# Kernel tuning notes

Hardware: AMD Instinct MI355X
Metric: run time of the kernel (lower is better)

## Reference

```python
import jax, jax.numpy as jnp
import numpy as np

H, W = 128, 128
TANX, TANY = 0.5, 0.5
SCALE_MOD = 1.0
N = 2048
T_EPS = 1e-4          # early-termination threshold used by the CUDA kernel
ALPHA_MIN = 1.0 / 255.0


def setup_inputs() -> dict:
    key = jax.random.key(0)
    ks = jax.random.split(key, 6)
    z = jax.random.uniform(ks[0], (N,), minval=2.0, maxval=6.0)
    xy = jax.random.uniform(ks[1], (N, 2), minval=-0.8, maxval=0.8) * (z[:, None] * TANX)
    means3D = jnp.concatenate([xy, z[:, None]], axis=1).astype(jnp.float32)
    means2D = jnp.zeros((N, 3), jnp.float32)  # gradient receptacle in the original API
    opacities = (jax.random.uniform(ks[2], (N, 1)) * 0.9 + 0.05).astype(jnp.float32)
    colors_precomp = jax.random.uniform(ks[3], (N, 3)).astype(jnp.float32)
    scales = jax.random.uniform(ks[4], (N, 3), minval=0.01, maxval=0.05).astype(jnp.float32)
    q = jax.random.normal(ks[5], (N, 4))
    rotations = (q / jnp.linalg.norm(q, axis=1, keepdims=True)).astype(jnp.float32)
    bg = jnp.zeros((3,), jnp.float32)
    viewmatrix = jnp.eye(4, dtype=jnp.float32)  # camera at origin looking +z (row-vector convention)
    znear, zfar = 0.01, 100.0
    P = np.zeros((4, 4), np.float32)
    P[0, 0] = 1.0 / TANX
    P[1, 1] = 1.0 / TANY
    P[2, 2] = zfar / (zfar - znear)
    P[2, 3] = -(zfar * znear) / (zfar - znear)
    P[3, 2] = 1.0
    projmatrix = jnp.asarray(P.T)  # full view@proj, row-vector convention
    return dict(bg=bg, means3D=means3D, means2D=means2D, opacities=opacities,
                colors_precomp=colors_precomp, scales=scales, rotations=rotations,
                viewmatrix=viewmatrix, projmatrix=projmatrix)


def _quat_to_rot(q):
    r, x, y, z = q[:, 0], q[:, 1], q[:, 2], q[:, 3]
    return jnp.stack([
        jnp.stack([1 - 2 * (y * y + z * z), 2 * (x * y - r * z), 2 * (x * z + r * y)], -1),
        jnp.stack([2 * (x * y + r * z), 1 - 2 * (x * x + z * z), 2 * (y * z - r * x)], -1),
        jnp.stack([2 * (x * z - r * y), 2 * (y * z + r * x), 1 - 2 * (x * x + y * y)], -1)], -2)


def _rasterize(bg, means3D, opacities, colors, scales, rotations, viewmatrix, projmatrix):
    n = means3D.shape[0]
    mh = jnp.concatenate([means3D, jnp.ones((n, 1), means3D.dtype)], 1)
    p_view = mh @ viewmatrix                 # [N,4] camera-space position
    tz = p_view[:, 2]
    p_hom = mh @ projmatrix
    p_proj = p_hom[:, :3] / (p_hom[:, 3:4] + 1e-7)
    # 3D covariance Sigma = (R S)(R S)^T
    qn = rotations / jnp.linalg.norm(rotations, axis=1, keepdims=True)
    Rm = _quat_to_rot(qn)
    M = Rm * (scales * SCALE_MOD)[:, None, :]      # R @ diag(s)
    Sigma = jnp.einsum('nij,nkj->nik', M, M)
    # EWA projection to a 2D covariance
    fx, fy = W / (2 * TANX), H / (2 * TANY)
    tx = jnp.clip(p_view[:, 0] / tz, -1.3 * TANX, 1.3 * TANX) * tz
    ty = jnp.clip(p_view[:, 1] / tz, -1.3 * TANY, 1.3 * TANY) * tz
    zero = jnp.zeros_like(tz)
    J = jnp.stack([jnp.stack([fx / tz, zero, -fx * tx / (tz * tz)], -1),
                   jnp.stack([zero, fy / tz, -fy * ty / (tz * tz)], -1)], -2)  # [N,2,3]
    Wr = viewmatrix[:3, :3]
    cov_cam = jnp.einsum('ji,njk,kl->nil', Wr, Sigma, Wr)      # W^T Sigma W
    cov2d = jnp.einsum('nij,njk,nlk->nil', J, cov_cam, J)      # [N,2,2]
    a = cov2d[:, 0, 0] + 0.3
    c = cov2d[:, 1, 1] + 0.3
    b = cov2d[:, 0, 1]
    det = a * c - b * b
    valid = (tz > 0.2) & (det > 0.0)                            # near-plane + degenerate culling
    det_s = jnp.where(det > 0.0, det, 1.0)
    conA, conB, conC = c / det_s, -b / det_s, a / det_s         # conic (inverse 2D cov)
    mid = 0.5 * (a + c)
    lam = mid + jnp.sqrt(jnp.maximum(0.1, mid * mid - det))
    radii = jnp.where(valid, jnp.ceil(3.0 * jnp.sqrt(lam)), 0.0).astype(jnp.int32)
    # NDC -> pixel coords
    px = ((p_proj[:, 0] + 1.0) * W - 1.0) * 0.5
    py = ((p_proj[:, 1] + 1.0) * H - 1.0) * 0.5
    # global front-to-back depth sort (per-tile in the CUDA kernel)
    order = jnp.argsort(tz)
    px_s, py_s = px[order], py[order]
    cA, cB, cC = conA[order], conB[order], conC[order]
    op_s = opacities[order, 0]
    col_s = colors[order]
    tz_s = tz[order]
    val_s = valid[order]
    yy, xx = jnp.meshgrid(jnp.arange(H, dtype=means3D.dtype),
                          jnp.arange(W, dtype=means3D.dtype), indexing='ij')
    gx, gy = xx.reshape(-1, 1), yy.reshape(-1, 1)   # [P,1]
    dx = px_s[None, :] - gx                          # [P,N]
    dy = py_s[None, :] - gy
    power = -0.5 * (cA[None, :] * dx * dx + cC[None, :] * dy * dy) - cB[None, :] * dx * dy
    alpha = jnp.minimum(0.99, op_s[None, :] * jnp.exp(power))
    alpha = jnp.where((power <= 0.0) & (alpha >= ALPHA_MIN) & val_s[None, :], alpha, 0.0)
    Tinc = jnp.cumprod(1.0 - alpha, axis=1)
    T = jnp.concatenate([jnp.ones((H * W, 1), alpha.dtype), Tinc[:, :-1]], axis=1)  # exclusive transmittance
    wgt = jnp.where(T > T_EPS, alpha * T, 0.0)       # early termination
    color = wgt @ col_s + Tinc[:, -1:] * bg[None, :]  # [P,3]
    depth = wgt @ tz_s                                # [P]
    counter = jnp.sum(wgt > 0.0, axis=1).astype(jnp.int32)
    color = color.reshape(H, W, 3).transpose(2, 0, 1)
    depth = depth.reshape(1, H, W)
    counter = counter.reshape(H, W)
    return color, depth, radii, counter


def reference(bg, means3D, means2D, opacities, colors_precomp, scales, rotations, viewmatrix, projmatrix):
    # means2D is only a gradient receptacle in the original API; it does not affect the math.
    return _rasterize(bg, means3D, opacities, colors_precomp, scales, rotations, viewmatrix, projmatrix)
```

## Files before the change

kernel.cpp:

```cpp
#include <hip/hip_runtime.h>
#include <math.h>

#define N_G   2048
#define W_IMG 128
#define H_IMG 128
#define NPIX  (W_IMG * H_IMG)
#define TANX  0.5f
#define TANY  0.5f
#define ALPHA_MIN (1.0f / 255.0f)
#define T_EPS_C 1e-4f
#define NTHR  1024
#define NWAVE 16
#define CAP   1024

__device__ __forceinline__ void full_chain(int i,
        const float* __restrict__ means3D, const float* __restrict__ opac,
        const float* __restrict__ colors, const float* __restrict__ scales,
        const float* __restrict__ rots, const float* __restrict__ viewm,
        const float* __restrict__ projm,
        float4& f1, float4& f2, float& radf) {
    float mx = means3D[i * 3 + 0], my = means3D[i * 3 + 1], mz = means3D[i * 3 + 2];
    float pv0 = mx * viewm[0] + my * viewm[4] + mz * viewm[8]  + viewm[12];
    float pv1 = mx * viewm[1] + my * viewm[5] + mz * viewm[9]  + viewm[13];
    float tz  = mx * viewm[2] + my * viewm[6] + mz * viewm[10] + viewm[14];

    float qr = rots[i * 4 + 0], qx = rots[i * 4 + 1], qy = rots[i * 4 + 2], qz = rots[i * 4 + 3];
    float qn = __builtin_amdgcn_rsqf(qr * qr + qx * qx + qy * qy + qz * qz);
    qr *= qn; qx *= qn; qy *= qn; qz *= qn;
    float R[3][3] = {
        {1.0f - 2.0f * (qy * qy + qz * qz), 2.0f * (qx * qy - qr * qz), 2.0f * (qx * qz + qr * qy)},
        {2.0f * (qx * qy + qr * qz), 1.0f - 2.0f * (qx * qx + qz * qz), 2.0f * (qy * qz - qr * qx)},
        {2.0f * (qx * qz - qr * qy), 2.0f * (qy * qz + qr * qx), 1.0f - 2.0f * (qx * qx + qy * qy)}};

    float sc[3] = {scales[i * 3 + 0], scales[i * 3 + 1], scales[i * 3 + 2]};
    float M[3][3];
#pragma unroll
    for (int r = 0; r < 3; r++)
#pragma unroll
        for (int cx = 0; cx < 3; cx++) M[r][cx] = R[r][cx] * sc[cx];

    float Sg[3][3];
#pragma unroll
    for (int r = 0; r < 3; r++)
#pragma unroll
        for (int kk = 0; kk < 3; kk++)
            Sg[r][kk] = M[r][0] * M[kk][0] + M[r][1] * M[kk][1] + M[r][2] * M[kk][2];

    float T1[3][3];
#pragma unroll
    for (int j = 0; j < 3; j++)
#pragma unroll
        for (int l = 0; l < 3; l++)
            T1[j][l] = Sg[j][0] * viewm[0 * 4 + l] + Sg[j][1] * viewm[1 * 4 + l] + Sg[j][2] * viewm[2 * 4 + l];
    float Cc[3][3];
#pragma unroll
    for (int r = 0; r < 3; r++)
#pragma unroll
        for (int l = 0; l < 3; l++)
            Cc[r][l] = viewm[0 * 4 + r] * T1[0][l] + viewm[1 * 4 + r] * T1[1][l] + viewm[2 * 4 + r] * T1[2][l];

    const float fx = W_IMG / (2.0f * TANX), fy = H_IMG / (2.0f * TANY);
    float invtz = __builtin_amdgcn_rcpf(tz);
    float txl = fminf(fmaxf(pv0 * invtz, -1.3f * TANX), 1.3f * TANX) * tz;
    float tyl = fminf(fmaxf(pv1 * invtz, -1.3f * TANY), 1.3f * TANY) * tz;
    float a0 = fx * invtz, a2 = -fx * txl * invtz * invtz;
    float b1 = fy * invtz, b2 = -fy * tyl * invtz * invtz;

    float c00 = a0 * a0 * Cc[0][0] + 2.0f * a0 * a2 * Cc[0][2] + a2 * a2 * Cc[2][2];
    float c11 = b1 * b1 * Cc[1][1] + 2.0f * b1 * b2 * Cc[1][2] + b2 * b2 * Cc[2][2];
    float c01 = a0 * b1 * Cc[0][1] + a0 * b2 * Cc[0][2] + a2 * b1 * Cc[1][2] + a2 * b2 * Cc[2][2];

    float a = c00 + 0.3f, c = c11 + 0.3f, b = c01;
    float det = a * c - b * b;
    bool valid = (tz > 0.2f) && (det > 0.0f);
    float det_s = (det > 0.0f) ? det : 1.0f;
    float rdet = __builtin_amdgcn_rcpf(det_s);
    float conA = c * rdet, conB = -b * rdet, conC = a * rdet;
    float mid = 0.5f * (a + c);
    float lam = mid + __builtin_amdgcn_sqrtf(fmaxf(0.1f, mid * mid - det));
    radf = valid ? ceilf(3.0f * __builtin_amdgcn_sqrtf(lam)) : 0.0f;

    float op = opac[i];
    f1 = make_float4(conA, conB, conC, valid ? op : 0.0f);
    f2 = make_float4(colors[i * 3 + 0], colors[i * 3 + 1], colors[i * 3 + 2], tz);
}

__global__ __launch_bounds__(NTHR) void gs_fused(const float* __restrict__ means3D,
                                                 const float* __restrict__ opac,
                                                 const float* __restrict__ colors,
                                                 const float* __restrict__ scales,
                                                 const float* __restrict__ rots,
                                                 const float* __restrict__ viewm,
                                                 const float* __restrict__ projm,
                                                 const float* __restrict__ bg,
                                                 float* __restrict__ out) {
    __shared__ float4 bbx[N_G];
    __shared__ float  tzv[N_G];
    __shared__ unsigned short lst[N_G];
    __shared__ float4 sf1[CAP];
    __shared__ float4 sf2[CAP];
    __shared__ float2 spos[CAP];
    __shared__ float4 scratch4[CAP / 4];
    __shared__ float4 accv[NTHR];
    __shared__ int s_count;

    float* scr = (float*)scratch4;
    int tid = threadIdx.x;
    int bid = blockIdx.x;
    float* radii_out = out + 4 * NPIX;
    if (tid == 0) s_count = 0;

    float cs0 = fabsf(viewm[0]) + fabsf(viewm[4]) + fabsf(viewm[8]);
    float cs1 = fabsf(viewm[1]) + fabsf(viewm[5]) + fabsf(viewm[9]);
    float cs2 = fabsf(viewm[2]) + fabsf(viewm[6]) + fabsf(viewm[10]);
    float rs0 = fabsf(viewm[0]) + fabsf(viewm[1]) + fabsf(viewm[2]);
    float rs1 = fabsf(viewm[4]) + fabsf(viewm[5]) + fabsf(viewm[6]);
    float rs2 = fabsf(viewm[8]) + fabsf(viewm[9]) + fabsf(viewm[10]);
    float wb2 = fmaxf(cs0, fmaxf(cs1, cs2)) * fmaxf(rs0, fmaxf(rs1, rs2));

#pragma unroll
    for (int k = 0; k < N_G / NTHR; k++) {
        int i = k * NTHR + tid;
        float mx = means3D[i * 3 + 0], my = means3D[i * 3 + 1], mz = means3D[i * 3 + 2];
        float pv0 = mx * viewm[0] + my * viewm[4] + mz * viewm[8]  + viewm[12];
        float pv1 = mx * viewm[1] + my * viewm[5] + mz * viewm[9]  + viewm[13];
        float tz  = mx * viewm[2] + my * viewm[6] + mz * viewm[10] + viewm[14];

        float ph[4];
#pragma unroll
        for (int j = 0; j < 4; j++)
            ph[j] = mx * projm[0 * 4 + j] + my * projm[1 * 4 + j] + mz * projm[2 * 4 + j] + projm[3 * 4 + j];
        float inv_w = __builtin_amdgcn_rcpf(ph[3] + 1e-7f);
        float px = ((ph[0] * inv_w + 1.0f) * (float)W_IMG - 1.0f) * 0.5f;
        float py = ((ph[1] * inv_w + 1.0f) * (float)H_IMG - 1.0f) * 0.5f;

        float s0 = scales[i * 3 + 0], s1 = scales[i * 3 + 1], s2 = scales[i * 3 + 2];
        float smax2 = fmaxf(s0 * s0, fmaxf(s1 * s1, s2 * s2));
        float op = opac[i];
        float L = __logf(255.0f * op);

        float invtz = __builtin_amdgcn_rcpf(tz);
        float ux = pv0 * invtz, uy = pv1 * invtz;
        float u2x = fminf(ux * ux, 0.4225f);
        float u2y = fminf(uy * uy, 0.4225f);
        float f2 = (W_IMG / (2.0f * TANX)) * invtz;
        f2 *= f2;
        float sw = smax2 * wb2;
        float abound = f2 * (1.0f + u2x) * sw + 0.3f;
        float cbound = f2 * (1.0f + u2y) * sw + 0.3f;
        float exb = __builtin_amdgcn_sqrtf(2.0f * L * abound) * 1.03f + 0.05f;
        float eyb = __builtin_amdgcn_sqrtf(2.0f * L * cbound) * 1.03f + 0.05f;
        if (!(tz > 0.2f) || !(L > 0.0f)) { exb = -1e9f; eyb = -1e9f; }

        bbx[i] = make_float4(px, py, exb, eyb);
        tzv[i] = tz;
    }
    __syncthreads();

    int tilex = bid & 15, tiley = bid >> 4;
    int wave = tid >> 6, lane = tid & 63;

    {
        float tx0 = (float)(tilex << 3), ty0 = (float)(tiley << 3);
        float tx1 = tx0 + 7.0f, ty1 = ty0 + 7.0f;
#pragma unroll
        for (int cc = 0; cc < 2; cc++) {
            int gi = (wave * 2 + cc) * 64 + lane;
            float4 b = bbx[gi];
            bool pred = (b.x >= tx0 - b.z) && (b.x <= tx1 + b.z) &&
                        (b.y >= ty0 - b.w) && (b.y <= ty1 + b.w);
            unsigned long long m = __ballot(pred);
            int n = (int)__popcll(m);
            int base = 0;
            if (lane == 0 && n) base = atomicAdd(&s_count, n);
            base = __shfl(base, 0);
            if (pred)
                lst[base + (int)__popcll(m & ((1ull << lane) - 1ull))] = (unsigned short)gi;
        }
    }
    __syncthreads();
    int c = min(s_count, CAP);

    for (int t = tid; t < c; t += NTHR) scr[t] = tzv[lst[t]];
    __syncthreads();

    for (int t = tid; t < c; t += NTHR) {
        int gi = lst[t];
        float my = scr[t];
        int rank = 0;
        int j = 0;
        for (; j + 4 <= c; j += 4) {
            float4 v = scratch4[j >> 2];
            int i0 = lst[j], i1 = lst[j + 1], i2 = lst[j + 2], i3 = lst[j + 3];
            rank += (v.x < my) || (v.x == my && i0 < gi);
            rank += (v.y < my) || (v.y == my && i1 < gi);
            rank += (v.z < my) || (v.z == my && i2 < gi);
            rank += (v.w < my) || (v.w == my && i3 < gi);
        }
        for (; j < c; j++) {
            float v = scr[j];
            rank += (v < my) || (v == my && lst[j] < gi);
        }
        float4 f1, f2v; float radf;
        full_chain(gi, means3D, opac, colors, scales, rots, viewm, projm, f1, f2v, radf);
        sf1[rank] = f1;
        sf2[rank] = f2v;
        float4 b = bbx[gi];
        spos[rank] = make_float2(b.x, b.y);
    }
    if (tid < 8) {
        int g8 = bid * 8 + tid;
        float4 d1, d2; float radf;
        full_chain(g8, means3D, opac, colors, scales, rots, viewm, projm, d1, d2, radf);
        radii_out[g8] = (float)(int)radf;
    }
    __syncthreads();

    float gx = (float)((tilex << 3) + (lane & 7));
    float gy = (float)((tiley << 3) + (lane >> 3));
    int seglen = (c + NWAVE - 1) / NWAVE;
    int s0 = wave * seglen;
    int s1 = min(c, s0 + seglen);

    float Tw = 1.0f;
    for (int t = s0; t < s1; ++t) {
        float4 f1 = sf1[t];
        float2 pp = spos[t];
        float dx = pp.x - gx, dy = pp.y - gy;
        float power = -0.5f * (f1.x * dx * dx + f1.z * dy * dy) - f1.y * dx * dy;
        if (power <= 0.0f) {
            float alpha = fminf(0.99f, f1.w * __expf(power));
            if (alpha >= ALPHA_MIN) Tw *= (1.0f - alpha);
        }
    }
    scr[wave * 64 + lane] = Tw;
    __syncthreads();

    float T0 = 1.0f;
#pragma unroll
    for (int s = 0; s < NWAVE - 1; ++s) if (s < wave) T0 *= scr[s * 64 + lane];
    float T = T0, cr = 0.0f, cg = 0.0f, cb = 0.0f, dep = 0.0f;
    int cnt = 0;
    if (!__all(T0 <= T_EPS_C)) {
        for (int t = s0; t < s1; ++t) {
            float4 f1 = sf1[t];
            float4 f2v = sf2[t];
            float2 pp = spos[t];
            float dx = pp.x - gx, dy = pp.y - gy;
            float power = -0.5f * (f1.x * dx * dx + f1.z * dy * dy) - f1.y * dx * dy;
            if (power <= 0.0f) {
                float alpha = fminf(0.99f, f1.w * __expf(power));
                if (alpha >= ALPHA_MIN) {
                    if (T > T_EPS_C) {
                        float w = alpha * T;
                        cr += w * f2v.x; cg += w * f2v.y; cb += w * f2v.z;
                        dep += w * f2v.w;
                        cnt++;
                    }
                    T *= (1.0f - alpha);
                    if (__all(T <= T_EPS_C)) break;
                }
            }
        }
    }
    accv[wave * 64 + lane] = make_float4(cr, cg, cb, dep);
    ((int*)lst)[wave * 64 + lane] = cnt;
    __syncthreads();

    if (tid < 64) {
        float crr = 0.0f, cgg = 0.0f, cbb = 0.0f, dpp = 0.0f, Tf = 1.0f;
        int cnt_t = 0;
        const int* an = (const int*)lst;
#pragma unroll
        for (int s = 0; s < NWAVE; ++s) {
            float4 a = accv[s * 64 + tid];
            crr += a.x; cgg += a.y; cbb += a.z; dpp += a.w;
            cnt_t += an[s * 64 + tid];
            Tf *= scr[s * 64 + tid];
        }
        crr += Tf * bg[0]; cgg += Tf * bg[1]; cbb += Tf * bg[2];

        int pid = ((tiley << 3) + (tid >> 3)) * W_IMG + (tilex << 3) + (tid & 7);
        out[0 * NPIX + pid] = crr;
        out[1 * NPIX + pid] = cgg;
        out[2 * NPIX + pid] = cbb;
        out[3 * NPIX + pid] = dpp;
        out[4 * NPIX + N_G + pid] = (float)cnt_t;
    }
}

extern "C" void kernel_launch(void* const* d_in, const int* in_sizes, int n_in,
                              void* d_out, int out_size, void* d_ws, size_t ws_size,
                              hipStream_t stream) {
    const float* bg      = (const float*)d_in[0];
    const float* means3D = (const float*)d_in[1];
    const float* opac    = (const float*)d_in[3];
    const float* colors  = (const float*)d_in[4];
    const float* scales  = (const float*)d_in[5];
    const float* rots    = (const float*)d_in[6];
    const float* viewm   = (const float*)d_in[7];
    const float* projm   = (const float*)d_in[8];

    gs_fused<<<256, NTHR, 0, stream>>>(means3D, opac, colors, scales, rots,
                                       viewm, projm, bg, (float*)d_out);
}
```

Before: 14.79 us.

## Cull in registers and rank candidates by packed depth-index 64-bit keys

Bounding-box culling now happens directly in registers during the per-Gaussian projection, which removes the full bbx/tzv shared arrays and one barrier. Each surviving candidate is stored as a packed 64-bit key (depth bits shifted left, Gaussian index in the low 16 bits) plus its 2D position. The rank sort then compares single u64 keys instead of float depth plus a tie-break on index, and this also drops the gather pass into scratch. Packing relies on depths being positive, so the float bit pattern orders correctly, and on the index fitting in 16 bits.

```diff
diff --git a/kernel.cpp b/kernel.cpp
--- a/kernel.cpp
+++ b/kernel.cpp
@@ -94,21 +94,25 @@
                                                  const float* __restrict__ projm,
                                                  const float* __restrict__ bg,
                                                  float* __restrict__ out) {
-    __shared__ float4 bbx[N_G];
-    __shared__ float  tzv[N_G];
-    __shared__ unsigned short lst[N_G];
+    __shared__ unsigned long long ckey[CAP];
+    __shared__ float2 cpos[CAP];
     __shared__ float4 sf1[CAP];
     __shared__ float4 sf2[CAP];
     __shared__ float2 spos[CAP];
-    __shared__ float4 scratch4[CAP / 4];
+    __shared__ float  tseg[NTHR];
     __shared__ float4 accv[NTHR];
     __shared__ int s_count;
 
-    float* scr = (float*)scratch4;
     int tid = threadIdx.x;
     int bid = blockIdx.x;
     float* radii_out = out + 4 * NPIX;
     if (tid == 0) s_count = 0;
+    __syncthreads();
+
+    int tilex = bid & 15, tiley = bid >> 4;
+    int wave = tid >> 6, lane = tid & 63;
+    float tx0 = (float)(tilex << 3), ty0 = (float)(tiley << 3);
+    float tx1 = tx0 + 7.0f, ty1 = ty0 + 7.0f;
 
     float cs0 = fabsf(viewm[0]) + fabsf(viewm[4]) + fabsf(viewm[8]);
     float cs1 = fabsf(viewm[1]) + fabsf(viewm[5]) + fabsf(viewm[9]);
@@ -119,8 +123,8 @@
     float wb2 = fmaxf(cs0, fmaxf(cs1, cs2)) * fmaxf(rs0, fmaxf(rs1, rs2));
 
 #pragma unroll
-    for (int k = 0; k < N_G / NTHR; k++) {
-        int i = k * NTHR + tid;
+    for (int cc = 0; cc < 2; cc++) {
+        int i = (wave * 2 + cc) * 64 + lane;
         float mx = means3D[i * 3 + 0], my = means3D[i * 3 + 1], mz = means3D[i * 3 + 2];
         float pv0 = mx * viewm[0] + my * viewm[4] + mz * viewm[8]  + viewm[12];
         float pv1 = mx * viewm[1] + my * viewm[5] + mz * viewm[9]  + viewm[13];
@@ -150,63 +154,45 @@
         float cbound = f2 * (1.0f + u2y) * sw + 0.3f;
         float exb = __builtin_amdgcn_sqrtf(2.0f * L * abound) * 1.03f + 0.05f;
         float eyb = __builtin_amdgcn_sqrtf(2.0f * L * cbound) * 1.03f + 0.05f;
-        if (!(tz > 0.2f) || !(L > 0.0f)) { exb = -1e9f; eyb = -1e9f; }
-
-        bbx[i] = make_float4(px, py, exb, eyb);
-        tzv[i] = tz;
-    }
-    __syncthreads();
-
-    int tilex = bid & 15, tiley = bid >> 4;
-    int wave = tid >> 6, lane = tid & 63;
-
-    {
-        float tx0 = (float)(tilex << 3), ty0 = (float)(tiley << 3);
-        float tx1 = tx0 + 7.0f, ty1 = ty0 + 7.0f;
-#pragma unroll
-        for (int cc = 0; cc < 2; cc++) {
-            int gi = (wave * 2 + cc) * 64 + lane;
-            float4 b = bbx[gi];
-            bool pred = (b.x >= tx0 - b.z) && (b.x <= tx1 + b.z) &&
-                        (b.y >= ty0 - b.w) && (b.y <= ty1 + b.w);
-            unsigned long long m = __ballot(pred);
-            int n = (int)__popcll(m);
-            int base = 0;
-            if (lane == 0 && n) base = atomicAdd(&s_count, n);
-            base = __shfl(base, 0);
-            if (pred)
-                lst[base + (int)__popcll(m & ((1ull << lane) - 1ull))] = (unsigned short)gi;
+        bool ok = (tz > 0.2f) && (L > 0.0f);
+
+        bool pred = ok && (px >= tx0 - exb) && (px <= tx1 + exb) &&
+                          (py >= ty0 - eyb) && (py <= ty1 + eyb);
+        unsigned long long m = __ballot(pred);
+        int n = (int)__popcll(m);
+        int base = 0;
+        if (lane == 0 && n) base = atomicAdd(&s_count, n);
+        base = __shfl(base, 0);
+        if (pred) {
+            int slot = base + (int)__popcll(m & ((1ull << lane) - 1ull));
+            if (slot < CAP) {
+                unsigned int tzb = __float_as_uint(tz);
+                ckey[slot] = ((unsigned long long)tzb << 16) | (unsigned int)i;
+                cpos[slot] = make_float2(px, py);
+            }
         }
     }
     __syncthreads();
     int c = min(s_count, CAP);
 
-    for (int t = tid; t < c; t += NTHR) scr[t] = tzv[lst[t]];
-    __syncthreads();
-
     for (int t = tid; t < c; t += NTHR) {
-        int gi = lst[t];
-        float my = scr[t];
+        unsigned long long mykey = ckey[t];
         int rank = 0;
         int j = 0;
-        for (; j + 4 <= c; j += 4) {
-            float4 v = scratch4[j >> 2];
-            int i0 = lst[j], i1 = lst[j + 1], i2 = lst[j + 2], i3 = lst[j + 3];
-            rank += (v.x < my) || (v.x == my && i0 < gi);
-            rank += (v.y < my) || (v.y == my && i1 < gi);
-            rank += (v.z < my) || (v.z == my && i2 < gi);
-            rank += (v.w < my) || (v.w == my && i3 < gi);
-        }
-        for (; j < c; j++) {
-            float v = scr[j];
-            rank += (v < my) || (v == my && lst[j] < gi);
-        }
+        const ulonglong2* k2 = (const ulonglong2*)ckey;
+        for (; j + 2 <= c; j += 2) {
+            ulonglong2 v = k2[j >> 1];
+            rank += (v.x < mykey);
+            rank += (v.y < mykey);
+        }
+        for (; j < c; j++) rank += (ckey[j] < mykey);
+
+        int gi = (int)(mykey & 0xFFFFull);
         float4 f1, f2v; float radf;
         full_chain(gi, means3D, opac, colors, scales, rots, viewm, projm, f1, f2v, radf);
         sf1[rank] = f1;
         sf2[rank] = f2v;
-        float4 b = bbx[gi];
-        spos[rank] = make_float2(b.x, b.y);
+        spos[rank] = cpos[t];
     }
     if (tid < 8) {
         int g8 = bid * 8 + tid;
@@ -233,12 +219,12 @@
             if (alpha >= ALPHA_MIN) Tw *= (1.0f - alpha);
         }
     }
-    scr[wave * 64 + lane] = Tw;
+    tseg[wave * 64 + lane] = Tw;
     __syncthreads();
 
     float T0 = 1.0f;
 #pragma unroll
-    for (int s = 0; s < NWAVE - 1; ++s) if (s < wave) T0 *= scr[s * 64 + lane];
+    for (int s = 0; s < NWAVE - 1; ++s) if (s < wave) T0 *= tseg[s * 64 + lane];
     float T = T0, cr = 0.0f, cg = 0.0f, cb = 0.0f, dep = 0.0f;
     int cnt = 0;
     if (!__all(T0 <= T_EPS_C)) {
@@ -264,19 +250,19 @@
         }
     }
     accv[wave * 64 + lane] = make_float4(cr, cg, cb, dep);
-    ((int*)lst)[wave * 64 + lane] = cnt;
+    ((int*)cpos)[wave * 64 + lane] = cnt;
     __syncthreads();
 
     if (tid < 64) {
         float crr = 0.0f, cgg = 0.0f, cbb = 0.0f, dpp = 0.0f, Tf = 1.0f;
         int cnt_t = 0;
-        const int* an = (const int*)lst;
+        const int* an = (const int*)cpos;
 #pragma unroll
         for (int s = 0; s < NWAVE; ++s) {
             float4 a = accv[s * 64 + tid];
             crr += a.x; cgg += a.y; cbb += a.z; dpp += a.w;
             cnt_t += an[s * 64 + tid];
-            Tf *= scr[s * 64 + tid];
+            Tf *= tseg[s * 64 + tid];
         }
         crr += Tf * bg[0]; cgg += Tf * bg[1]; cbb += Tf * bg[2];
 
```

Result: no change. 14.95 us (+1.1%).
